# Kernel tuning notes

Measured on AMD Instinct MI355X. Metric: run time of the kernel, lower is better.

The kernel has to match this reference:

```python
import jax, jax.numpy as jnp
import numpy as np

NEG = -1e30  # log-space 'zero' that keeps gradients finite (vs -inf)


def setup_inputs() -> dict:
    key = jax.random.key(0)
    k1, k2, k3, k4 = jax.random.split(key, 4)
    B, T, V, S = 32, 2048, 128, 256
    predictions = jax.random.normal(k1, (B, T, V), dtype=jnp.float32)
    # input lengths in [T//2, T]; target lengths in [S//4, S]; labels in [1, V) (0 is blank)
    prediction_lengths = jax.random.randint(k2, (B,), T // 2, T + 1, dtype=jnp.int32)
    ground_truths = jax.random.randint(k3, (B, S), 1, V, dtype=jnp.int32)
    ground_truth_lengths = jax.random.randint(k4, (B,), S // 4, S + 1, dtype=jnp.int32)
    return {
        "predictions": predictions,
        "prediction_lengths": prediction_lengths,
        "ground_truths": ground_truths,
        "ground_truth_lengths": ground_truth_lengths,
    }


def _ctc_loss(log_probs, targets, input_lengths, target_lengths, blank=0):
    # log_probs: [T, B, V]; targets: [B, S]
    T, B, V = log_probs.shape
    S = targets.shape[1]
    L = 2 * S + 1  # extended label sequence: blank, l1, blank, l2, ..., blank
    ext = jnp.full((B, L), blank, dtype=targets.dtype).at[:, 1::2].set(targets)
    # skip transition s-2 -> s allowed iff ext[s] != blank and ext[s] != ext[s-2]
    skip = jnp.concatenate(
        [jnp.zeros((B, 2), dtype=bool), (ext[:, 2:] != blank) & (ext[:, 2:] != ext[:, :-2])],
        axis=1,
    )
    # gather per-extended-label log-probs: [T, B, L]
    lp_ext = jnp.take_along_axis(log_probs, jnp.broadcast_to(ext[None], (T, B, L)), axis=2)

    alpha0 = (
        jnp.full((B, L), NEG, dtype=log_probs.dtype)
        .at[:, 0].set(lp_ext[0, :, 0])
        .at[:, 1].set(lp_ext[0, :, 1])
    )

    def step(alpha, lp_t):
        a1 = alpha
        a2 = jnp.pad(alpha[:, :-1], ((0, 0), (1, 0)), constant_values=NEG)
        a3 = jnp.where(skip, jnp.pad(alpha[:, :-2], ((0, 0), (2, 0)), constant_values=NEG), NEG)
        m = jnp.maximum(jnp.maximum(a1, a2), a3)
        new = m + jnp.log(jnp.exp(a1 - m) + jnp.exp(a2 - m) + jnp.exp(a3 - m)) + lp_t
        return new, new

    _, alphas = jax.lax.scan(step, alpha0, lp_ext[1:])
    alphas = jnp.concatenate([alpha0[None], alphas], axis=0)  # [T, B, L]

    bidx = jnp.arange(B)
    alpha_final = alphas[input_lengths - 1, bidx]  # [B, L] at each sequence's last frame
    last = 2 * target_lengths  # index of final blank; last-1 is final label
    loss = -jnp.logaddexp(alpha_final[bidx, last], alpha_final[bidx, last - 1])
    loss = jnp.where(loss < 1e10, loss, 0.0)  # zero_infinity=True
    # torch reduction='mean': per-sample loss / target_length, then batch mean
    return (loss / target_lengths.astype(loss.dtype)).mean()


def reference(predictions, prediction_lengths, ground_truths, ground_truth_lengths):
    # module: transpose to [T, B, V], log_softmax over vocab, then CTC loss
    log_probs = jax.nn.log_softmax(jnp.transpose(predictions, (1, 0, 2)), axis=2)
    return _ctc_loss(log_probs, ground_truths, prediction_lengths, ground_truth_lengths, blank=0)
```

## Files before the change

kernel.cpp:

```cpp
#include <hip/hip_runtime.h>
#include <math.h>

constexpr int V = 128;

__device__ __forceinline__ double dpp_shr1_f64(double x) {
    int lo = __builtin_amdgcn_update_dpp(0, __double2loint(x), 0x138, 0xf, 0xf, false);
    int hi = __builtin_amdgcn_update_dpp(0, __double2hiint(x), 0x138, 0xf, 0xf, false);
    return __hiloint2double(hi, lo);
}
__device__ __forceinline__ double dpp_shl1_f64(double x) {
    int lo = __builtin_amdgcn_update_dpp(0, __double2loint(x), 0x130, 0xf, 0xf, false);
    int hi = __builtin_amdgcn_update_dpp(0, __double2hiint(x), 0x130, 0xf, 0xf, false);
    return __hiloint2double(hi, lo);
}

__global__ __launch_bounds__(256) void ctc_prelude(
    const float* __restrict__ pred, const int* __restrict__ gt,
    const int* __restrict__ gt_len, const int* __restrict__ pred_len,
    float* __restrict__ g, float* __restrict__ z, float* __restrict__ x0a,
    int T, int S)
{
    int wid  = blockIdx.x * 4 + (threadIdx.x >> 6);
    int lane = threadIdx.x & 63;
    int w4   = threadIdx.x >> 6;
    int b    = wid / T;
    int t    = wid - b * T;
    if (t >= pred_len[b]) return;
    __shared__ float rows[4][V];

    const float2* p = (const float2*)pred + (size_t)wid * 64;
    float2 v = p[lane];
    rows[w4][2 * lane]     = v.x;
    rows[w4][2 * lane + 1] = v.y;
    float x0 = __shfl(v.x, 0, 64);
    float s = __expf(v.x) + __expf(v.y);
    #pragma unroll
    for (int off = 32; off >= 1; off >>= 1) s += __shfl_xor(s, off, 64);
    if (lane == 0) { z[wid] = __logf(s); x0a[wid] = v.x; }

    int4 la = *(const int4*)(gt + b * S + 4 * lane);
    int tl = gt_len[b];
    float4 o;
    o.x = (4 * lane + 0 < tl) ? __expf(rows[w4][la.x] - x0) : 0.f;
    o.y = (4 * lane + 1 < tl) ? __expf(rows[w4][la.y] - x0) : 0.f;
    o.z = (4 * lane + 2 < tl) ? __expf(rows[w4][la.z] - x0) : 0.f;
    o.w = (4 * lane + 3 < tl) ? __expf(rows[w4][la.w] - x0) : 0.f;
    *(float4*)(g + (size_t)wid * 256 + 4 * lane) = o;
}

__global__ __launch_bounds__(64) void ctc_scan_bi(
    const float* __restrict__ g,
    const int*   __restrict__ pred_len,
    const int*   __restrict__ gt,
    const int*   __restrict__ gt_len,
    double*      __restrict__ fwdv,
    double*      __restrict__ bwdv,
    int*         __restrict__ Kf,
    int*         __restrict__ Kb,
    int T, int S)
{
    const int blk  = blockIdx.x;
    const int b    = blk >> 1;
    const int dir  = blk & 1;
    const int lane = threadIdx.x;
    const int len  = pred_len[b];
    const int tl   = gt_len[b];
    const int L    = 2 * tl + 1;
    const int m    = (len + 1) >> 1;

    int4 la = *(const int4*)(gt + b * S + 4 * lane);
    int law_up = __shfl_up(la.w, 1, 64);
    int lax_dn = __shfl_down(la.x, 1, 64);
    const double sk0 = (lane > 0 && la.x != law_up) ? 1.0 : 0.0;
    const double sk1 = (la.y != la.x) ? 1.0 : 0.0;
    const double sk2 = (la.z != la.y) ? 1.0 : 0.0;
    const double sk3 = (la.w != la.z) ? 1.0 : 0.0;
    const double sk4 = (lax_dn != la.w) ? 1.0 : 0.0;

    const char* gb = (const char*)(g + (size_t)b * T * 256) + lane * 16;

    float4 raw[16];
    double u[9];
    int K = 0;

    auto RESCALE = [&]() {
        double mx = u[0];
        #pragma unroll
        for (int j = 1; j < 9; ++j) mx = fmax(mx, u[j]);
        #pragma unroll
        for (int off = 32; off >= 1; off >>= 1)
            mx = fmax(mx, __shfl_xor(mx, off, 64));
        int k = ((__double2hiint(mx) >> 20) & 0x7ff) - 1023;
        #pragma unroll
        for (int j = 0; j < 9; ++j) u[j] = ldexp(u[j], -k);
        K += k;
    };

    if (dir == 0) {
        #pragma unroll
        for (int i = 0; i < 16; ++i)
            raw[i] = *(const float4*)(gb + (size_t)i * 1024);
        #pragma unroll
        for (int j = 0; j < 9; ++j) u[j] = 0.0;
        if (lane == 0) { u[0] = 1.0; u[1] = (double)raw[0].x; }
        raw[0] = *(const float4*)(gb + (size_t)16 * 1024);
        const char* pf = gb + (size_t)17 * 1024;

        auto FSTEP = [&](int i) {
            float4 g4 = raw[i];
            raw[i] = *(const float4*)pf; pf += 1024;
            double um1 = dpp_shr1_f64(u[7]);
            double gx = (double)g4.x, gy = (double)g4.y;
            double gz = (double)g4.z, gw = (double)g4.w;
            u[8] = u[8] + u[7];
            u[7] = (fma(sk3, u[5], u[6]) + u[7]) * gw;
            u[6] = u[6] + u[5];
            u[5] = (fma(sk2, u[3], u[4]) + u[5]) * gz;
            u[4] = u[4] + u[3];
            u[3] = (fma(sk1, u[1], u[2]) + u[3]) * gy;
            u[2] = u[2] + u[1];
            u[1] = (fma(sk0, um1, u[0]) + u[1]) * gx;
            u[0] = u[0] + um1;
        };

        #pragma unroll
        for (int t = 1; t < 16; ++t) FSTEP(t);
        int tb = 16;
        for (; tb + 16 <= m; tb += 16) {
            #pragma unroll
            for (int i = 0; i < 16; ++i) FSTEP(i);
            if (((tb + 16) & 63) == 0) RESCALE();
        }
        #pragma unroll
        for (int i = 0; i < 15; ++i)
            if (tb + i < m) FSTEP(i);
        RESCALE();

        double* outv = fwdv + (size_t)b * 520;
        #pragma unroll
        for (int j = 0; j < 8; ++j) outv[8 * lane + j] = u[j];
        if (lane == 63) outv[512] = u[8];
        if (lane == 0)  Kf[b] = K;
    } else {
        const int nb = len - m;
        #pragma unroll
        for (int i = 0; i < 16; ++i)
            raw[i] = *(const float4*)(gb + (size_t)(len - 1 - i) * 1024);
        #pragma unroll
        for (int j = 0; j < 8; ++j) {
            int s = 8 * lane + j;
            u[j] = (s == 2 * tl || s == 2 * tl - 1) ? 1.0 : 0.0;
        }
        u[8] = (L == 513) ? 1.0 : 0.0;
        const char* pf = gb + (size_t)(len - 17) * 1024;

        auto BSTEP = [&](int i) {
            float4 g4 = raw[i];
            raw[i] = *(const float4*)pf; pf -= 1024;
            double d0 = dpp_shl1_f64(u[0]);
            if (lane == 63) d0 = u[8];
            double p1 = (double)g4.x * u[1], p3 = (double)g4.y * u[3];
            double p5 = (double)g4.z * u[5], p7 = (double)g4.w * u[7];
            double dp = dpp_shl1_f64(p1);
            u[0] = u[0] + p1;
            u[1] = fma(sk1, p3, u[2]) + p1;
            u[2] = u[2] + p3;
            u[3] = fma(sk2, p5, u[4]) + p3;
            u[4] = u[4] + p5;
            u[5] = fma(sk3, p7, u[6]) + p5;
            u[6] = u[6] + p7;
            u[7] = fma(sk4, dp, d0) + p7;
        };

        #pragma unroll
        for (int k = 0; k < 16; ++k) BSTEP(k);
        int kb = 16;
        for (; kb + 16 <= nb; kb += 16) {
            #pragma unroll
            for (int i = 0; i < 16; ++i) BSTEP(i);
            if (((kb + 16) & 63) == 0) RESCALE();
        }
        #pragma unroll
        for (int i = 0; i < 15; ++i)
            if (kb + i < nb) BSTEP(i);
        RESCALE();

        double* outv = bwdv + (size_t)b * 520;
        #pragma unroll
        for (int j = 0; j < 8; ++j) outv[8 * lane + j] = u[j];
        if (lane == 63) outv[512] = u[8];
        if (lane == 0)  Kb[b] = K;
    }
}

__global__ __launch_bounds__(64) void ctc_combine(
    const double* __restrict__ fwdv, const double* __restrict__ bwdv,
    const int* __restrict__ Kf, const int* __restrict__ Kb,
    const float* __restrict__ z, const float* __restrict__ x0a,
    const int* __restrict__ pred_len, const int* __restrict__ gt_len,
    float* __restrict__ lossb, int T)
{
    int b = blockIdx.x, lane = threadIdx.x;
    int len = pred_len[b], tl = gt_len[b];
    const double* f = fwdv + (size_t)b * 520;
    const double* w = bwdv + (size_t)b * 520;
    double c = 0.0;
    #pragma unroll
    for (int j = 0; j < 8; ++j)
        c = fma(f[8 * lane + j], w[8 * lane + j], c);
    if (lane == 63) c = fma(f[512], w[512], c);
    #pragma unroll
    for (int off = 32; off >= 1; off >>= 1) c += __shfl_xor(c, off, 64);

    double zs = 0.0;
    for (int t = lane; t < len; t += 64)
        zs += (double)z[b * T + t] - (double)x0a[b * T + t];
    #pragma unroll
    for (int off = 32; off >= 1; off >>= 1) zs += __shfl_xor(zs, off, 64);

    if (lane == 0) {
        double logp = log(c)
                    + (double)(Kf[b] + Kb[b]) * 0.6931471805599453 - zs;
        double loss = -logp;
        if (!(loss < 1e10)) loss = 0.0;
        lossb[b] = (float)(loss / (double)tl);
    }
}

__global__ void ctc_reduce_kernel(const float* __restrict__ ls,
                                  float* __restrict__ out, int B)
{
    if (blockIdx.x == 0 && threadIdx.x == 0) {
        float s = 0.0f;
        for (int i = 0; i < B; ++i) s += ls[i];
        out[0] = s / (float)B;
    }
}

constexpr int SPL  = 9;
constexpr int RING = 32;

__global__ __launch_bounds__(256) void softmax_z_kernel(
    const float* __restrict__ pred, float* __restrict__ z, int nrows)
{
    int w    = blockIdx.x * 4 + (threadIdx.x >> 6);
    int lane = threadIdx.x & 63;
    if (w >= nrows) return;
    const float2* p = (const float2*)pred;
    float2 v = p[(size_t)w * 64 + lane];
    float s = __expf(v.x) + __expf(v.y);
    #pragma unroll
    for (int off = 32; off >= 1; off >>= 1) s += __shfl_xor(s, off, 64);
    if (lane == 0) z[w] = __logf(s);
}

__device__ __forceinline__ void ctc_step_fb(
    const float* __restrict__ rowbase, const int* __restrict__ goff,
    const double* __restrict__ skd, double (&u)[SPL], int lane)
{
    float gf[SPL];
    #pragma unroll
    for (int j = 0; j < SPL; ++j)
        gf[j] = *(const float*)((const char*)rowbase + goff[j]);
    double um1 = __shfl_up(u[8], 1, 64);
    double um2 = __shfl_up(u[7], 1, 64);
    if (lane == 0) { um1 = 0.0; um2 = 0.0; }
    #pragma unroll
    for (int jj = 0; jj < SPL; ++jj) {
        int j = SPL - 1 - jj;
        double a2 = (j >= 1) ? u[j - 1] : um1;
        double a3 = (j >= 2) ? u[j - 2] : ((j == 1) ? um1 : um2);
        double t  = fma(skd[j], a3, a2) + u[j];
        u[j] = t * (double)gf[j];
    }
}

__device__ __forceinline__ void ctc_rescale_fb(double (&u)[SPL], int& K)
{
    double m = u[0];
    #pragma unroll
    for (int j = 1; j < SPL; ++j) m = fmax(m, u[j]);
    #pragma unroll
    for (int off = 32; off >= 1; off >>= 1) m = fmax(m, __shfl_xor(m, off, 64));
    if (m > 0.0) {
        int e = (__double2hiint(m) >> 20) & 0x7ff;
        int k = e - 1023;
        #pragma unroll
        for (int j = 0; j < SPL; ++j) u[j] = ldexp(u[j], -k);
        K += k;
    }
}

__global__ __launch_bounds__(64) void ctc_scan_kernel(
    const float* __restrict__ pred, const int* __restrict__ pred_len,
    const int* __restrict__ gt, const int* __restrict__ gt_len,
    const float* __restrict__ z, float* __restrict__ loss_out, int T, int S)
{
    const int b    = blockIdx.x;
    const int lane = threadIdx.x;
    const int len  = pred_len[b];
    const int tl   = gt_len[b];
    const int L    = 2 * tl + 1;

    __shared__ float ring[RING][V];
    __shared__ int   gts[512];

    for (int i = lane; i < S; i += 64) gts[i] = gt[b * S + i];
    __syncthreads();

    int    goff[SPL];
    double skd[SPL];
    #pragma unroll
    for (int j = 0; j < SPL; ++j) {
        int s = SPL * lane + j;
        int e = 0, ep = 0;
        if (s < L && (s & 1)) e = gts[s >> 1];
        if (s >= 2 && s < L && (s & 1)) ep = gts[(s - 2) >> 1];
        goff[j] = e * 4;
        skd[j]  = (s >= 2 && s < L && e != 0 && e != ep) ? 1.0 : 0.0;
    }

    const float2* rowp = (const float2*)(pred + (size_t)b * T * V);
    float2 raw[16];

    #pragma unroll
    for (int i = 0; i < 16; ++i) raw[i] = rowp[(size_t)i * 64 + lane];
    #pragma unroll
    for (int i = 0; i < 16; ++i) {
        float2 w; w.x = __expf(raw[i].x); w.y = __expf(raw[i].y);
        *(float2*)&ring[i][2 * lane] = w;
    }
    #pragma unroll
    for (int i = 0; i < 16; ++i) raw[i] = rowp[(size_t)(16 + i) * 64 + lane];
    #pragma unroll
    for (int i = 0; i < 16; ++i) {
        float2 w; w.x = __expf(raw[i].x); w.y = __expf(raw[i].y);
        *(float2*)&ring[16 + i][2 * lane] = w;
    }
    #pragma unroll
    for (int i = 0; i < 16; ++i) {
        int r = 32 + i; if (r > T - 1) r = T - 1;
        raw[i] = rowp[(size_t)r * 64 + lane];
    }

    double u[SPL];
    #pragma unroll
    for (int j = 0; j < SPL; ++j) {
        int s = SPL * lane + j;
        float w0 = *(const float*)((const char*)&ring[0][0] + goff[j]);
        u[j] = (s < 2) ? (double)w0 : 0.0;
    }
    int K = 0;

    for (int t = 1; t < 16 && t < len; ++t)
        ctc_step_fb(&ring[t & (RING - 1)][0], goff, skd, u, lane);
    ctc_rescale_fb(u, K);

    int tb = 16;
    for (; tb + 16 <= len; tb += 16) {
        #pragma unroll
        for (int i = 0; i < 16; ++i) {
            float2 w; w.x = __expf(raw[i].x); w.y = __expf(raw[i].y);
            *(float2*)&ring[(tb + 16 + i) & (RING - 1)][2 * lane] = w;
        }
        #pragma unroll
        for (int i = 0; i < 16; ++i) {
            int r = tb + 32 + i; if (r > T - 1) r = T - 1;
            raw[i] = rowp[(size_t)r * 64 + lane];
        }
        #pragma unroll
        for (int i = 0; i < 16; ++i)
            ctc_step_fb(&ring[(tb + i) & (RING - 1)][0], goff, skd, u, lane);
        ctc_rescale_fb(u, K);
    }

    for (int t = tb; t < len; ++t)
        ctc_step_fb(&ring[t & (RING - 1)][0], goff, skd, u, lane);

    double contrib = 0.0;
    #pragma unroll
    for (int j = 0; j < SPL; ++j) {
        int s = SPL * lane + j;
        if (s == L - 1 || s == L - 2) contrib += u[j];
    }
    #pragma unroll
    for (int off = 32; off >= 1; off >>= 1)
        contrib += __shfl_xor(contrib, off, 64);

    double zsum = 0.0;
    for (int t = lane; t < len; t += 64) zsum += (double)z[b * T + t];
    #pragma unroll
    for (int off = 32; off >= 1; off >>= 1)
        zsum += __shfl_xor(zsum, off, 64);

    if (lane == 0) {
        double lg    = log(contrib);
        double alpha = lg + (double)K * 0.6931471805599453 - zsum;
        double loss  = -alpha;
        if (!(loss < 1e10)) loss = 0.0;
        loss_out[b] = (float)(loss / (double)tl);
    }
}

extern "C" void kernel_launch(void* const* d_in, const int* in_sizes, int n_in,
                              void* d_out, int out_size, void* d_ws, size_t ws_size,
                              hipStream_t stream) {
    const float* pred = (const float*)d_in[0];
    const int*   plen = (const int*)d_in[1];
    const int*   gts  = (const int*)d_in[2];
    const int*   glen = (const int*)d_in[3];

    const int B = in_sizes[1];
    const int S = in_sizes[2] / B;
    const int T = in_sizes[0] / (B * V);
    const size_t BT = (size_t)B * T;

    float* out = (float*)d_out;
    char*  ws  = (char*)d_ws;

    size_t off_z   = 0;
    size_t off_x0  = off_z   + BT * 4;
    size_t off_lb  = off_x0  + BT * 4;
    size_t off_fw  = (off_lb + (size_t)B * 4 + 255) & ~(size_t)255;
    size_t off_bw  = off_fw  + (size_t)B * 520 * 8;
    size_t off_kf  = off_bw  + (size_t)B * 520 * 8;
    size_t off_kb  = off_kf  + (size_t)B * 4;
    size_t off_g   = (off_kb + (size_t)B * 4 + 1023) & ~(size_t)1023;
    size_t need    = off_g + BT * 256 * 4;

    bool fast_ok = (ws_size >= need) && (S == 256) && (T % 4 == 0) &&
                   (T >= 96) && (B <= 32);

    if (fast_ok) {
        float*  zp  = (float*)(ws + off_z);
        float*  x0a = (float*)(ws + off_x0);
        float*  lb  = (float*)(ws + off_lb);
        double* fw  = (double*)(ws + off_fw);
        double* bw  = (double*)(ws + off_bw);
        int*    kf  = (int*)(ws + off_kf);
        int*    kb  = (int*)(ws + off_kb);
        float*  g   = (float*)(ws + off_g);

        ctc_prelude<<<B * T / 4, 256, 0, stream>>>(pred, gts, glen, plen,
                                                   g, zp, x0a, T, S);
        ctc_scan_bi<<<2 * B, 64, 0, stream>>>(g, plen, gts, glen,
                                              fw, bw, kf, kb, T, S);
        ctc_combine<<<B, 64, 0, stream>>>(fw, bw, kf, kb, zp, x0a,
                                          plen, glen, lb, T);
        ctc_reduce_kernel<<<1, 64, 0, stream>>>(lb, out, B);
    } else {
        float* zbuf = (float*)ws;
        float* lb   = zbuf + BT;
        int nrows = B * T;
        softmax_z_kernel<<<(nrows + 3) / 4, 256, 0, stream>>>(pred, zbuf, nrows);
        ctc_scan_kernel<<<B, 64, 0, stream>>>(pred, plen, gts, glen, zbuf, lb, T, S);
        ctc_reduce_kernel<<<1, 64, 0, stream>>>(lb, out, B);
    }
}
```

Measured before the change: 174.8 us.

## Fuse combine and final reduction into bidirectional scan via atomic completion counters

Removes the separate combine and reduce kernel launches. The forward and backward scan blocks each signal a per-batch atomic counter, and the second block to finish does the combine for that sample. A global counter then lets the last sample's finisher compute the batch mean. This saves two kernel launches and their gaps, at the cost of an extra memset launch, fences and atomics, and it widens the fast path to B up to 64.

```diff
diff --git a/kernel.cpp b/kernel.cpp
--- a/kernel.cpp
+++ b/kernel.cpp
@@ -53,11 +53,15 @@
     const int*   __restrict__ pred_len,
     const int*   __restrict__ gt,
     const int*   __restrict__ gt_len,
+    const float* __restrict__ z,
+    const float* __restrict__ x0a,
     double*      __restrict__ fwdv,
     double*      __restrict__ bwdv,
     int*         __restrict__ Kf,
     int*         __restrict__ Kb,
-    int T, int S)
+    int* done, int* gdone, float* lossb,
+    float* __restrict__ out,
+    int T, int S, int B)
 {
     const int blk  = blockIdx.x;
     const int b    = blk >> 1;
@@ -191,17 +195,16 @@
         if (lane == 63) outv[512] = u[8];
         if (lane == 0)  Kb[b] = K;
     }
-}
-
-__global__ __launch_bounds__(64) void ctc_combine(
-    const double* __restrict__ fwdv, const double* __restrict__ bwdv,
-    const int* __restrict__ Kf, const int* __restrict__ Kb,
-    const float* __restrict__ z, const float* __restrict__ x0a,
-    const int* __restrict__ pred_len, const int* __restrict__ gt_len,
-    float* __restrict__ lossb, int T)
-{
-    int b = blockIdx.x, lane = threadIdx.x;
-    int len = pred_len[b], tl = gt_len[b];
+
+    __threadfence();
+    int prev = 0;
+    if (lane == 0)
+        prev = __hip_atomic_fetch_add(&done[b], 1, __ATOMIC_ACQ_REL,
+                                      __HIP_MEMORY_SCOPE_AGENT);
+    prev = __shfl(prev, 0, 64);
+    if (prev == 0) return;
+    __threadfence();
+
     const double* f = fwdv + (size_t)b * 520;
     const double* w = bwdv + (size_t)b * 520;
     double c = 0.0;
@@ -224,8 +227,20 @@
         double loss = -logp;
         if (!(loss < 1e10)) loss = 0.0;
         lossb[b] = (float)(loss / (double)tl);
-    }
-}
+        __threadfence();
+        int pg = __hip_atomic_fetch_add(gdone, 1, __ATOMIC_ACQ_REL,
+                                        __HIP_MEMORY_SCOPE_AGENT);
+        if (pg == B - 1) {
+            __threadfence();
+            float ssum = 0.0f;
+            for (int i = 0; i < B; ++i) ssum += lossb[i];
+            out[0] = ssum / (float)B;
+        }
+    }
+}
+
+constexpr int SPL  = 9;
+constexpr int RING = 32;
 
 __global__ void ctc_reduce_kernel(const float* __restrict__ ls,
                                   float* __restrict__ out, int B)
@@ -236,9 +251,6 @@
         out[0] = s / (float)B;
     }
 }
-
-constexpr int SPL  = 9;
-constexpr int RING = 32;
 
 __global__ __launch_bounds__(256) void softmax_z_kernel(
     const float* __restrict__ pred, float* __restrict__ z, int nrows)
@@ -418,10 +430,10 @@
     float* out = (float*)d_out;
     char*  ws  = (char*)d_ws;
 
-    size_t off_z   = 0;
+    size_t off_fl  = 0;
+    size_t off_z   = 1024;
     size_t off_x0  = off_z   + BT * 4;
-    size_t off_lb  = off_x0  + BT * 4;
-    size_t off_fw  = (off_lb + (size_t)B * 4 + 255) & ~(size_t)255;
+    size_t off_fw  = (off_x0 + BT * 4 + 255) & ~(size_t)255;
     size_t off_bw  = off_fw  + (size_t)B * 520 * 8;
     size_t off_kf  = off_bw  + (size_t)B * 520 * 8;
     size_t off_kb  = off_kf  + (size_t)B * 4;
@@ -429,25 +441,26 @@
     size_t need    = off_g + BT * 256 * 4;
 
     bool fast_ok = (ws_size >= need) && (S == 256) && (T % 4 == 0) &&
-                   (T >= 96) && (B <= 32);
+                   (T >= 96) && (B >= 1) && (B <= 64);
 
     if (fast_ok) {
-        float*  zp  = (float*)(ws + off_z);
-        float*  x0a = (float*)(ws + off_x0);
-        float*  lb  = (float*)(ws + off_lb);
-        double* fw  = (double*)(ws + off_fw);
-        double* bw  = (double*)(ws + off_bw);
-        int*    kf  = (int*)(ws + off_kf);
-        int*    kb  = (int*)(ws + off_kb);
-        float*  g   = (float*)(ws + off_g);
-
+        int*    done  = (int*)(ws + off_fl);
+        int*    gdone = (int*)(ws + off_fl + 256);
+        float*  lossb = (float*)(ws + off_fl + 512);
+        float*  zp    = (float*)(ws + off_z);
+        float*  x0a   = (float*)(ws + off_x0);
+        double* fw    = (double*)(ws + off_fw);
+        double* bw    = (double*)(ws + off_bw);
+        int*    kf    = (int*)(ws + off_kf);
+        int*    kb    = (int*)(ws + off_kb);
+        float*  g     = (float*)(ws + off_g);
+
+        hipMemsetAsync(ws + off_fl, 0, 512, stream);
         ctc_prelude<<<B * T / 4, 256, 0, stream>>>(pred, gts, glen, plen,
                                                    g, zp, x0a, T, S);
-        ctc_scan_bi<<<2 * B, 64, 0, stream>>>(g, plen, gts, glen,
-                                              fw, bw, kf, kb, T, S);
-        ctc_combine<<<B, 64, 0, stream>>>(fw, bw, kf, kb, zp, x0a,
-                                          plen, glen, lb, T);
-        ctc_reduce_kernel<<<1, 64, 0, stream>>>(lb, out, B);
+        ctc_scan_bi<<<2 * B, 64, 0, stream>>>(g, plen, gts, glen, zp, x0a,
+                                              fw, bw, kf, kb,
+                                              done, gdone, lossb, out, T, S, B);
     } else {
         float* zbuf = (float*)ws;
         float* lb   = zbuf + BT;
```

New measurement: 173.4 us. About the same (-0.8%).
